# Performance work log

Measured on AMD Instinct MI355X. Metric: run time of the kernel, lower is better.

Reference implementation:

```python
import jax, jax.numpy as jnp
import numpy as np

DIL = 1  # dilation (== padding for 3x3 stride-1)
KK = 9   # 3x3 kernel points


def setup_inputs() -> dict:
    key = jax.random.key(0)
    k1, k2, k3, k4 = jax.random.split(key, 4)
    B, C, H, W = 8, 64, 128, 128
    Cout = 64
    x = jax.random.normal(k1, (B, C, H, W), jnp.float32)
    # offset/mask conv: nn.Conv2d default init scale-ish; keep offsets moderate
    w_off = jax.random.normal(k2, (27, C, 3, 3), jnp.float32) * 0.02
    b_off = jax.random.uniform(k3, (27,), jnp.float32, -0.05, 0.05)
    # c2_msra_fill: std = sqrt(2 / (fan_in + fan_out)), fan_in = C*9
    std = float(np.sqrt(2.0 / (C * 9 + Cout)))
    w_dcn = jax.random.normal(k4, (Cout, C, 3, 3), jnp.float32) * std
    return {"x": x, "w_off": w_off, "b_off": b_off, "w_dcn": w_dcn}


def _conv3x3(x, w, b, dil):
    out = jax.lax.conv_general_dilated(
        x, w, window_strides=(1, 1), padding=[(dil, dil), (dil, dil)],
        rhs_dilation=(dil, dil), dimension_numbers=("NCHW", "OIHW", "NCHW"))
    return out + b[None, :, None, None]


def reference(x, w_off, b_off, w_dcn):
    B, C, H, W = x.shape
    Cout = w_dcn.shape[0]
    # offset/mask conv, chunk into offset_x / offset_y / mask, cat offsets
    om = _conv3x3(x, w_off, b_off, DIL)                  # [B,27,H,W]
    off_x, off_y, mask = jnp.split(om, 3, axis=1)        # each [B,9,H,W]
    offset = jnp.concatenate([off_x, off_y], axis=1)     # [B,18,H,W]
    mask = jax.nn.sigmoid(mask)                          # [B,9,H,W]
    # mmcv DCNv2 layout: offset channel 2k = dy_k, 2k+1 = dx_k
    off = offset.reshape(B, KK, 2, H, W)
    dy, dx = off[:, :, 0], off[:, :, 1]                  # [B,9,H,W]
    # base sampling grid: p = out_pos - pad + k*dil (stride 1, pad = dil)
    ky, kx = jnp.meshgrid(jnp.arange(3), jnp.arange(3), indexing="ij")
    ky = ky.reshape(KK).astype(jnp.float32)
    kx = kx.reshape(KK).astype(jnp.float32)
    base_y = (jnp.arange(H, dtype=jnp.float32)[None, :, None]
              - DIL + ky[:, None, None] * DIL)           # [9,H,1]
    base_x = (jnp.arange(W, dtype=jnp.float32)[None, None, :]
              - DIL + kx[:, None, None] * DIL)           # [9,1,W]
    py = dy + base_y[None]                               # [B,9,H,W]
    px = dx + base_x[None]
    # bilinear sample with zero padding outside the image
    y0 = jnp.floor(py)
    x0 = jnp.floor(px)
    xf = x.reshape(B, C, H * W)
    sampled = jnp.zeros((B, C, KK, H, W), x.dtype)
    for oy in (0.0, 1.0):
        for ox in (0.0, 1.0):
            yi = y0 + oy
            xi = x0 + ox
            wgt = (1.0 - jnp.abs(py - yi)) * (1.0 - jnp.abs(px - xi))
            valid = (yi >= 0) & (yi < H) & (xi >= 0) & (xi < W)
            yc = jnp.clip(yi, 0, H - 1).astype(jnp.int32)
            xc = jnp.clip(xi, 0, W - 1).astype(jnp.int32)
            idx = (yc * W + xc).reshape(B, KK * H * W)
            vals = jax.vmap(lambda f, i: jnp.take(f, i, axis=1))(xf, idx)
            vals = vals.reshape(B, C, KK, H, W)
            sampled = sampled + vals * (wgt * valid)[:, None]
    sampled = sampled * mask[:, None]                    # modulation
    # weighted reduction == conv with gathered patches
    out = jnp.einsum("bckhw,ock->bohw", sampled, w_dcn.reshape(Cout, C, KK))
    return out
```

## Files before the change

kernel.cpp:

```cpp
#include <hip/hip_runtime.h>
#include <math.h>

#define B_  8
#define C_  64
#define H_  128
#define W_  128
#define KK_ 9
#define CO_ 64
#define HW_ (H_*W_)
#define CK_ 576

typedef _Float16 f16x8 __attribute__((ext_vector_type(8)));
typedef _Float16 h2    __attribute__((ext_vector_type(2)));
typedef __attribute__((ext_vector_type(4))) float f32x4;

__device__ inline unsigned pkrtz(float a, float b){
    auto v = __builtin_amdgcn_cvt_pkrtz(a, b);
    union{decltype(v) h; unsigned u;} c; c.h = v; return c.u;
}
__device__ inline h2 u2h(unsigned u){ union{unsigned x; h2 h;} c; c.x = u; return c.h; }
__device__ inline unsigned h2u(h2 v){ union{h2 h; unsigned u;} c; c.h = v; return c.u; }
__device__ inline unsigned short f2h(float f){
    _Float16 h = (_Float16)f;
    union{_Float16 h; unsigned short s;} c; c.h = h; return c.s;
}
__device__ inline h2 bcast_lo(unsigned u){ return u2h(__builtin_amdgcn_perm(u, u, 0x01000100)); }
__device__ inline h2 bcast_hi(unsigned u){ return u2h(__builtin_amdgcn_perm(u, u, 0x03020302)); }

__global__ __launch_bounds__(256) void transpose_prep(
    const float* __restrict__ x, unsigned short* __restrict__ xt,
    const float* __restrict__ w_dcn, const float* __restrict__ w_off,
    unsigned short* __restrict__ w_bf, unsigned short* __restrict__ wA)
{
    __shared__ unsigned tb[64 * 33];
    if (blockIdx.x >= B_ * 256) {
        int i = (blockIdx.x - B_ * 256) * 256 + threadIdx.x;
        if (i < 64 * CK_) {
            int o = i / CK_, r = i % CK_;
            int tap = r >> 6, c = r & 63;
            w_bf[i] = f2h(w_dcn[o * CK_ + c * 9 + tap]);
        } else {
            int j = i - 64 * CK_;
            int o = j / CK_, r = j % CK_;
            int tap = r >> 6, c = r & 63;
            float v = (o < 27) ? w_off[o * CK_ + c * 9 + tap] : 0.f;
            wA[j] = f2h(v);
        }
        return;
    }
    int b = blockIdx.x >> 8;
    int pixbase = (blockIdx.x & 255) * 64;
    int t = threadIdx.x;
    #pragma unroll
    for (int i = 0; i < 2; ++i) {
        int idx = i * 256 + t;
        int cp = idx >> 4;
        int p4 = (idx & 15) * 4;
        const float* r0 = x + ((size_t)(b * C_) + 2 * cp    ) * HW_ + pixbase + p4;
        const float* r1 = x + ((size_t)(b * C_) + 2 * cp + 1) * HW_ + pixbase + p4;
        float4 f0 = *(const float4*)r0;
        float4 f1 = *(const float4*)r1;
        tb[(p4 + 0) * 33 + cp] = pkrtz(f0.x, f1.x);
        tb[(p4 + 1) * 33 + cp] = pkrtz(f0.y, f1.y);
        tb[(p4 + 2) * 33 + cp] = pkrtz(f0.z, f1.z);
        tb[(p4 + 3) * 33 + cp] = pkrtz(f0.w, f1.w);
    }
    __syncthreads();
    unsigned* xo = (unsigned*)xt + ((size_t)b * HW_ + pixbase) * 32;
    #pragma unroll
    for (int i = 0; i < 2; ++i) {
        int idx = i * 256 + t;
        int pix = idx >> 3, j = idx & 7;
        uint4 v;
        v.x = tb[pix * 33 + j * 4 + 0];
        v.y = tb[pix * 33 + j * 4 + 1];
        v.z = tb[pix * 33 + j * 4 + 2];
        v.w = tb[pix * 33 + j * 4 + 3];
        *(uint4*)(xo + pix * 32 + j * 4) = v;
    }
}

#define SSTR4 400
__global__ __launch_bounds__(256, 5) void dcn12(
    const unsigned short* __restrict__ xt,
    const unsigned short* __restrict__ wA,
    const float* __restrict__ b_off,
    const unsigned short* __restrict__ w_bf,
    float* __restrict__ out)
{
    __shared__ __align__(16) unsigned char sS[64 * SSTR4];
    __shared__ uint2 scr_w[576];
    __shared__ int   scr_o[576];
    float* om = (float*)sS;

    int tile = blockIdx.x;
    int b  = tile >> 8;
    int p0 = (tile & 255) * 64;
    int y  = p0 >> 7;
    int x0 = p0 & 127;
    int t  = threadIdx.x;
    int lane = t & 63, w = t >> 6;
    int m = lane & 15, q = lane >> 4;

    const unsigned short* xbr = xt + (size_t)(b * HW_) * 64;

    {
        int o0c = (w & 1) * 16;
        int pxh = (w >> 1) * 32;

        f32x4 accc[2] = {};
        #pragma unroll
        for (int ky = 0; ky < 3; ++ky) {
            int yy = y + ky - 1;
            if (yy >= 0 && yy < H_) {
                const unsigned short* xr = xbr + (size_t)yy * W_ * 64;
                #pragma unroll
                for (int kx = 0; kx < 3; ++kx) {
                    int s2 = (ky * 3 + kx) * 2;
                    f16x8 A0 = *(const f16x8*)(wA + (o0c + m) * CK_ + s2 * 32 + q * 8);
                    f16x8 A1 = *(const f16x8*)(wA + (o0c + m) * CK_ + (s2 + 1) * 32 + q * 8);
                    #pragma unroll
                    for (int nt = 0; nt < 2; ++nt) {
                        int xbase = x0 + pxh + nt * 16;
                        int px = xbase + m + kx - 1;
                        f16x8 b0, b1;
                        bool ledge = (xbase == 0   && kx == 0);
                        bool redge = (xbase == 112 && kx == 2);
                        if (ledge || redge) {
                            int pc = min(max(px, 0), W_ - 1);
                            const unsigned short* p = xr + pc * 64 + q * 8;
                            b0 = *(const f16x8*)p;
                            b1 = *(const f16x8*)(p + 32);
                            if (px != pc) {
                                b0 = (f16x8){0,0,0,0,0,0,0,0};
                                b1 = (f16x8){0,0,0,0,0,0,0,0};
                            }
                        } else {
                            const unsigned short* p = xr + px * 64 + q * 8;
                            b0 = *(const f16x8*)p;
                            b1 = *(const f16x8*)(p + 32);
                        }
                        accc[nt] = __builtin_amdgcn_mfma_f32_16x16x32_f16(A0, b0, accc[nt], 0, 0, 0);
                        accc[nt] = __builtin_amdgcn_mfma_f32_16x16x32_f16(A1, b1, accc[nt], 0, 0, 0);
                    }
                }
            }
        }
        #pragma unroll
        for (int nt = 0; nt < 2; ++nt) {
            #pragma unroll
            for (int r = 0; r < 4; ++r) {
                int j = o0c + q * 4 + r;
                if (j < 27)
                    om[j * 65 + pxh + nt * 16 + m] = accc[nt][r] + b_off[j];
            }
        }
    }
    __syncthreads();

    for (int i = t; i < 576; i += 256) {
        int k = i >> 6, sp = i & 63;
        float dy = om[(2 * k)     * 65 + sp];
        float dx = om[(2 * k + 1) * 65 + sp];
        float mk = 1.f / (1.f + __expf(-om[(18 + k) * 65 + sp]));
        float py = dy + (float)(y - 1 + k / 3);
        float px = dx + (float)(x0 + sp - 1 + k % 3);
        float fy = floorf(py), fx = floorf(px);
        int iy = (int)fy, ix = (int)fx;
        float ay = py - fy, ax = px - fx;
        float wy0 = (iy >= 0  && iy < H_)     ? (1.f - ay) : 0.f;
        float wy1 = (iy >= -1 && iy < H_ - 1) ? ay         : 0.f;
        float wx0 = (ix >= 0  && ix < W_)     ? (1.f - ax) : 0.f;
        float wx1 = (ix >= -1 && ix < W_ - 1) ? ax         : 0.f;
        int iy0 = min(max(iy, 0), H_ - 1);
        int iy1 = min(max(iy + 1, 0), H_ - 1);
        int ix0 = min(max(ix, 0), W_ - 1);
        int ix1 = min(max(ix + 1, 0), W_ - 1);
        float w00 = wy0*wx0*mk, w01 = wy0*wx1*mk, w10 = wy1*wx0*mk, w11 = wy1*wx1*mk;
        uint2 wv;
        wv.x = pkrtz(w00, w01);
        wv.y = pkrtz(w10, w11);
        scr_w[i] = wv;
        int off00 = (iy0 * W_ + ix0) * 128;
        scr_o[i] = off00 | ((ix1 != ix0) << 22) | ((iy1 != iy0) << 23);
    }

    int o0 = w * 16;
    __syncthreads();

    int cq = lane & 7;
    int g  = lane >> 3;
    const unsigned char* xb = (const unsigned char*)xbr;
    f32x4 acc[4] = {};
    int piB = w * 8 + g;

    uint2 wA_, wB_; int pB_;
    uint4 a00, a01, a10, a11;
    {
        wA_ = scr_w[piB];      int oo = scr_o[piB];
        wB_ = scr_w[piB + 32]; pB_ = scr_o[piB + 32];
        const unsigned char* a0 = xb + (oo & 0x3FFFFF) + cq * 16;
        int dxb = (oo >> 15) & 128;
        int dyb = (oo >> 9)  & 16384;
        a00 = *(const uint4*)(a0);
        a01 = *(const uint4*)(a0 + dxb);
        a10 = *(const uint4*)(a0 + dyb);
        a11 = *(const uint4*)(a0 + dyb + dxb);
    }

    #pragma unroll
    for (int chunk = 0; chunk < 3; ++chunk) {
        #pragma unroll
        for (int it6 = 0; it6 < 6; ++it6) {
            const int k = chunk * 6 + it6;
            uint2 wC_ = {}; int pC_ = 0;
            if (k + 2 < 18) {
                int P = piB + (k + 2) * 32;
                wC_ = scr_w[P]; pC_ = scr_o[P];
            }
            uint4 n00 = {}, n01 = {}, n10 = {}, n11 = {};
            if (k + 1 < 18) {
                const unsigned char* a0 = xb + (pB_ & 0x3FFFFF) + cq * 16;
                int dxb = (pB_ >> 15) & 128;
                int dyb = (pB_ >> 9)  & 16384;
                n00 = *(const uint4*)(a0);
                n01 = *(const uint4*)(a0 + dxb);
                n10 = *(const uint4*)(a0 + dyb);
                n11 = *(const uint4*)(a0 + dyb + dxb);
            }
            h2 w00 = bcast_lo(wA_.x), w01 = bcast_hi(wA_.x);
            h2 w10 = bcast_lo(wA_.y), w11 = bcast_hi(wA_.y);
            uint4 o4; h2 r;
            r = w00*u2h(a00.x) + w01*u2h(a01.x) + w10*u2h(a10.x) + w11*u2h(a11.x); o4.x = h2u(r);
            r = w00*u2h(a00.y) + w01*u2h(a01.y) + w10*u2h(a10.y) + w11*u2h(a11.y); o4.y = h2u(r);
            r = w00*u2h(a00.z) + w01*u2h(a01.z) + w10*u2h(a10.z) + w11*u2h(a11.z); o4.z = h2u(r);
            r = w00*u2h(a00.w) + w01*u2h(a01.w) + w10*u2h(a10.w) + w11*u2h(a11.w); o4.w = h2u(r);
            int sp  = (piB + (k & 1) * 32) & 63;
            int ktl = it6 >> 1;
            *(uint4*)&sS[sp * SSTR4 + ktl * 128 + cq * 16] = o4;
            wA_ = wB_; wB_ = wC_; pB_ = pC_;
            a00 = n00; a01 = n01; a10 = n10; a11 = n11;
        }
        f16x8 Af[6];
        #pragma unroll
        for (int s = 0; s < 6; ++s)
            Af[s] = *(const f16x8*)(w_bf + (o0 + m) * CK_ + (chunk * 6 + s) * 32 + q * 8);
        __syncthreads();

        #pragma unroll
        for (int s = 0; s < 6; ++s) {
            #pragma unroll
            for (int nt = 0; nt < 4; ++nt) {
                f16x8 bb = *(const f16x8*)&sS[(nt * 16 + m) * SSTR4 + s * 64 + q * 16];
                acc[nt] = __builtin_amdgcn_mfma_f32_16x16x32_f16(Af[s], bb, acc[nt], 0, 0, 0);
            }
        }
        __syncthreads();
    }

    #pragma unroll
    for (int nt = 0; nt < 4; ++nt) {
        #pragma unroll
        for (int r = 0; r < 4; ++r) {
            int o = o0 + q * 4 + r;
            out[((size_t)(b * CO_ + o)) * HW_ + p0 + nt * 16 + m] = acc[nt][r];
        }
    }
}

extern "C" void kernel_launch(void* const* d_in, const int* in_sizes, int n_in,
                              void* d_out, int out_size, void* d_ws, size_t ws_size,
                              hipStream_t stream)
{
    const float* x     = (const float*)d_in[0];
    const float* w_off = (const float*)d_in[1];
    const float* b_off = (const float*)d_in[2];
    const float* w_dcn = (const float*)d_in[3];
    float* out = (float*)d_out;

    unsigned short* xt   = (unsigned short*)d_ws;
    unsigned short* w_bf = xt + (size_t)B_ * HW_ * 64;
    unsigned short* wA   = w_bf + 64 * CK_;

    transpose_prep<<<B_ * 256 + 216, 256, 0, stream>>>(x, xt, w_dcn, w_off, w_bf, wA);
    dcn12<<<B_ * 256, 256, 0, stream>>>(xt, wA, b_off, w_bf, out);
}
```

Baseline: 173.5 us.

## Feed bilinear samples directly into MFMA registers instead of staging through LDS

Each wave now samples its own 16 pixels per tap and builds the MFMA B operand directly in registers, which removes the shared-memory staging buffer and the two barriers per chunk. Every wave then computes all 64 output channels for its 16 pixels, so each wave loads the full weight matrix from global memory instead of a 16-row slice. The explicit software prefetch of the next tap's gathers is dropped. Occupancy hint is lowered from 5 to 4 blocks per CU, and shared memory use shrinks to the offset buffer plus scratch.

```diff
diff --git a/kernel.cpp b/kernel.cpp
--- a/kernel.cpp
+++ b/kernel.cpp
@@ -80,18 +80,16 @@
     }
 }
 
-#define SSTR4 400
-__global__ __launch_bounds__(256, 5) void dcn12(
+__global__ __launch_bounds__(256, 4) void dcn13(
     const unsigned short* __restrict__ xt,
     const unsigned short* __restrict__ wA,
     const float* __restrict__ b_off,
     const unsigned short* __restrict__ w_bf,
     float* __restrict__ out)
 {
-    __shared__ __align__(16) unsigned char sS[64 * SSTR4];
+    __shared__ __align__(16) float om[27 * 65];
     __shared__ uint2 scr_w[576];
     __shared__ int   scr_o[576];
-    float* om = (float*)sS;
 
     int tile = blockIdx.x;
     int b  = tile >> 8;
@@ -184,86 +182,57 @@
         int off00 = (iy0 * W_ + ix0) * 128;
         scr_o[i] = off00 | ((ix1 != ix0) << 22) | ((iy1 != iy0) << 23);
     }
-
-    int o0 = w * 16;
     __syncthreads();
 
-    int cq = lane & 7;
-    int g  = lane >> 3;
+    int px = w * 16 + m;
     const unsigned char* xb = (const unsigned char*)xbr;
     f32x4 acc[4] = {};
-    int piB = w * 8 + g;
-
-    uint2 wA_, wB_; int pB_;
-    uint4 a00, a01, a10, a11;
-    {
-        wA_ = scr_w[piB];      int oo = scr_o[piB];
-        wB_ = scr_w[piB + 32]; pB_ = scr_o[piB + 32];
-        const unsigned char* a0 = xb + (oo & 0x3FFFFF) + cq * 16;
+
+    #pragma unroll
+    for (int tap = 0; tap < 9; ++tap) {
+        uint2 wv = scr_w[tap * 64 + px];
+        int   oo = scr_o[tap * 64 + px];
+        const unsigned char* a0 = xb + (oo & 0x3FFFFF) + q * 16;
         int dxb = (oo >> 15) & 128;
         int dyb = (oo >> 9)  & 16384;
-        a00 = *(const uint4*)(a0);
-        a01 = *(const uint4*)(a0 + dxb);
-        a10 = *(const uint4*)(a0 + dyb);
-        a11 = *(const uint4*)(a0 + dyb + dxb);
-    }
-
-    #pragma unroll
-    for (int chunk = 0; chunk < 3; ++chunk) {
-        #pragma unroll
-        for (int it6 = 0; it6 < 6; ++it6) {
-            const int k = chunk * 6 + it6;
-            uint2 wC_ = {}; int pC_ = 0;
-            if (k + 2 < 18) {
-                int P = piB + (k + 2) * 32;
-                wC_ = scr_w[P]; pC_ = scr_o[P];
-            }
-            uint4 n00 = {}, n01 = {}, n10 = {}, n11 = {};
-            if (k + 1 < 18) {
-                const unsigned char* a0 = xb + (pB_ & 0x3FFFFF) + cq * 16;
-                int dxb = (pB_ >> 15) & 128;
-                int dyb = (pB_ >> 9)  & 16384;
-                n00 = *(const uint4*)(a0);
-                n01 = *(const uint4*)(a0 + dxb);
-                n10 = *(const uint4*)(a0 + dyb);
-                n11 = *(const uint4*)(a0 + dyb + dxb);
-            }
-            h2 w00 = bcast_lo(wA_.x), w01 = bcast_hi(wA_.x);
-            h2 w10 = bcast_lo(wA_.y), w11 = bcast_hi(wA_.y);
-            uint4 o4; h2 r;
-            r = w00*u2h(a00.x) + w01*u2h(a01.x) + w10*u2h(a10.x) + w11*u2h(a11.x); o4.x = h2u(r);
-            r = w00*u2h(a00.y) + w01*u2h(a01.y) + w10*u2h(a10.y) + w11*u2h(a11.y); o4.y = h2u(r);
-            r = w00*u2h(a00.z) + w01*u2h(a01.z) + w10*u2h(a10.z) + w11*u2h(a11.z); o4.z = h2u(r);
-            r = w00*u2h(a00.w) + w01*u2h(a01.w) + w10*u2h(a10.w) + w11*u2h(a11.w); o4.w = h2u(r);
-            int sp  = (piB + (k & 1) * 32) & 63;
-            int ktl = it6 >> 1;
-            *(uint4*)&sS[sp * SSTR4 + ktl * 128 + cq * 16] = o4;
-            wA_ = wB_; wB_ = wC_; pB_ = pC_;
-            a00 = n00; a01 = n01; a10 = n10; a11 = n11;
-        }
-        f16x8 Af[6];
-        #pragma unroll
-        for (int s = 0; s < 6; ++s)
-            Af[s] = *(const f16x8*)(w_bf + (o0 + m) * CK_ + (chunk * 6 + s) * 32 + q * 8);
-        __syncthreads();
-
-        #pragma unroll
-        for (int s = 0; s < 6; ++s) {
-            #pragma unroll
-            for (int nt = 0; nt < 4; ++nt) {
-                f16x8 bb = *(const f16x8*)&sS[(nt * 16 + m) * SSTR4 + s * 64 + q * 16];
-                acc[nt] = __builtin_amdgcn_mfma_f32_16x16x32_f16(Af[s], bb, acc[nt], 0, 0, 0);
-            }
-        }
-        __syncthreads();
-    }
-
-    #pragma unroll
-    for (int nt = 0; nt < 4; ++nt) {
+        uint4 cA0 = *(const uint4*)(a0);
+        uint4 cA1 = *(const uint4*)(a0 + dxb);
+        uint4 cA2 = *(const uint4*)(a0 + dyb);
+        uint4 cA3 = *(const uint4*)(a0 + dyb + dxb);
+        uint4 cB0 = *(const uint4*)(a0 + 64);
+        uint4 cB1 = *(const uint4*)(a0 + 64 + dxb);
+        uint4 cB2 = *(const uint4*)(a0 + 64 + dyb);
+        uint4 cB3 = *(const uint4*)(a0 + 64 + dyb + dxb);
+
+        h2 w00 = bcast_lo(wv.x), w01 = bcast_hi(wv.x);
+        h2 w10 = bcast_lo(wv.y), w11 = bcast_hi(wv.y);
+
+        union { uint4 u; f16x8 h; } f0, f1;
+        f0.u.x = h2u(w00*u2h(cA0.x) + w01*u2h(cA1.x) + w10*u2h(cA2.x) + w11*u2h(cA3.x));
+        f0.u.y = h2u(w00*u2h(cA0.y) + w01*u2h(cA1.y) + w10*u2h(cA2.y) + w11*u2h(cA3.y));
+        f0.u.z = h2u(w00*u2h(cA0.z) + w01*u2h(cA1.z) + w10*u2h(cA2.z) + w11*u2h(cA3.z));
+        f0.u.w = h2u(w00*u2h(cA0.w) + w01*u2h(cA1.w) + w10*u2h(cA2.w) + w11*u2h(cA3.w));
+        f1.u.x = h2u(w00*u2h(cB0.x) + w01*u2h(cB1.x) + w10*u2h(cB2.x) + w11*u2h(cB3.x));
+        f1.u.y = h2u(w00*u2h(cB0.y) + w01*u2h(cB1.y) + w10*u2h(cB2.y) + w11*u2h(cB3.y));
+        f1.u.z = h2u(w00*u2h(cB0.z) + w01*u2h(cB1.z) + w10*u2h(cB2.z) + w11*u2h(cB3.z));
+        f1.u.w = h2u(w00*u2h(cB0.w) + w01*u2h(cB1.w) + w10*u2h(cB2.w) + w11*u2h(cB3.w));
+
+        const unsigned short* wb = w_bf + tap * 64 + q * 8;
+        #pragma unroll
+        for (int jo = 0; jo < 4; ++jo) {
+            f16x8 A0 = *(const f16x8*)(wb + (jo * 16 + m) * CK_);
+            f16x8 A1 = *(const f16x8*)(wb + (jo * 16 + m) * CK_ + 32);
+            acc[jo] = __builtin_amdgcn_mfma_f32_16x16x32_f16(A0, f0.h, acc[jo], 0, 0, 0);
+            acc[jo] = __builtin_amdgcn_mfma_f32_16x16x32_f16(A1, f1.h, acc[jo], 0, 0, 0);
+        }
+    }
+
+    #pragma unroll
+    for (int jo = 0; jo < 4; ++jo) {
         #pragma unroll
         for (int r = 0; r < 4; ++r) {
-            int o = o0 + q * 4 + r;
-            out[((size_t)(b * CO_ + o)) * HW_ + p0 + nt * 16 + m] = acc[nt][r];
+            int o = jo * 16 + q * 4 + r;
+            out[((size_t)(b * CO_ + o)) * HW_ + p0 + w * 16 + m] = acc[jo][r];
         }
     }
 }
@@ -283,5 +252,5 @@
     unsigned short* wA   = w_bf + 64 * CK_;
 
     transpose_prep<<<B_ * 256 + 216, 256, 0, stream>>>(x, xt, w_dcn, w_off, w_bf, wA);
-    dcn12<<<B_ * 256, 256, 0, stream>>>(xt, wA, b_off, w_bf, out);
-}
+    dcn13<<<B_ * 256, 256, 0, stream>>>(xt, wA, b_off, w_bf, out);
+}
```

New measurement: 262.6 us. 1.51x slower.

## Split fused DCN kernel into offset-conv and sampling-GEMM kernels via workspace

Applied to the files above, without the earlier changes.

Splits the fused kernel in two. The first computes the offset/mask conv and writes per-tap bilinear weights and offsets (16 bytes per record) to a global workspace. The second reloads them into shared memory and runs the gather plus MFMA reduction. The goal is to lower register and LDS pressure per kernel and improve occupancy, at the cost of an extra launch and a global round trip of about 9.4 MB.

```diff
diff --git a/kernel.cpp b/kernel.cpp
--- a/kernel.cpp
+++ b/kernel.cpp
@@ -80,19 +80,14 @@
     }
 }
 
-#define SSTR4 400
-__global__ __launch_bounds__(256, 5) void dcn12(
+
+__global__ __launch_bounds__(256) void dcn_p1(
     const unsigned short* __restrict__ xt,
     const unsigned short* __restrict__ wA,
     const float* __restrict__ b_off,
-    const unsigned short* __restrict__ w_bf,
-    float* __restrict__ out)
+    uint4* __restrict__ scr_ws)
 {
-    __shared__ __align__(16) unsigned char sS[64 * SSTR4];
-    __shared__ uint2 scr_w[576];
-    __shared__ int   scr_o[576];
-    float* om = (float*)sS;
-
+    __shared__ __align__(16) float om[27 * 65];
     int tile = blockIdx.x;
     int b  = tile >> 8;
     int p0 = (tile & 255) * 64;
@@ -158,6 +153,7 @@
     }
     __syncthreads();
 
+    uint4* srow = scr_ws + (size_t)tile * 576;
     for (int i = t; i < 576; i += 256) {
         int k = i >> 6, sp = i & 63;
         float dy = om[(2 * k)     * 65 + sp];
@@ -177,14 +173,42 @@
         int ix0 = min(max(ix, 0), W_ - 1);
         int ix1 = min(max(ix + 1, 0), W_ - 1);
         float w00 = wy0*wx0*mk, w01 = wy0*wx1*mk, w10 = wy1*wx0*mk, w11 = wy1*wx1*mk;
-        uint2 wv;
-        wv.x = pkrtz(w00, w01);
-        wv.y = pkrtz(w10, w11);
-        scr_w[i] = wv;
+        uint4 rec;
+        rec.x = pkrtz(w00, w01);
+        rec.y = pkrtz(w10, w11);
         int off00 = (iy0 * W_ + ix0) * 128;
-        scr_o[i] = off00 | ((ix1 != ix0) << 22) | ((iy1 != iy0) << 23);
-    }
-
+        rec.z = (unsigned)(off00 | ((ix1 != ix0) << 22) | ((iy1 != iy0) << 23));
+        rec.w = 0;
+        srow[i] = rec;
+    }
+}
+
+#define SSTR4 400
+__global__ __launch_bounds__(256, 4) void dcn_p2(
+    const unsigned short* __restrict__ xt,
+    const unsigned short* __restrict__ w_bf,
+    const uint4* __restrict__ scr_ws,
+    float* __restrict__ out)
+{
+    __shared__ __align__(16) unsigned char sS[64 * SSTR4];
+    __shared__ uint2 scr_w[576];
+    __shared__ int   scr_o[576];
+
+    int tile = blockIdx.x;
+    int b  = tile >> 8;
+    int p0 = (tile & 255) * 64;
+    int t  = threadIdx.x;
+    int lane = t & 63, w = t >> 6;
+    int m = lane & 15, q = lane >> 4;
+
+    const unsigned short* xbr = xt + (size_t)(b * HW_) * 64;
+
+    const uint4* srow = scr_ws + (size_t)tile * 576;
+    for (int i = t; i < 576; i += 256) {
+        uint4 rec = srow[i];
+        scr_w[i] = (uint2){rec.x, rec.y};
+        scr_o[i] = (int)rec.z;
+    }
     int o0 = w * 16;
     __syncthreads();
 
@@ -281,7 +305,9 @@
     unsigned short* xt   = (unsigned short*)d_ws;
     unsigned short* w_bf = xt + (size_t)B_ * HW_ * 64;
     unsigned short* wA   = w_bf + 64 * CK_;
+    uint4* scr_ws = (uint4*)(wA + 32 * CK_);
 
     transpose_prep<<<B_ * 256 + 216, 256, 0, stream>>>(x, xt, w_dcn, w_off, w_bf, wA);
-    dcn12<<<B_ * 256, 256, 0, stream>>>(xt, wA, b_off, w_bf, out);
-}
+    dcn_p1<<<B_ * 256, 256, 0, stream>>>(xt, wA, b_off, scr_ws);
+    dcn_p2<<<B_ * 256, 256, 0, stream>>>(xt, w_bf, scr_ws, out);
+}
```

Result: slower. 181.2 us (+4.4%).
